# Performance work log

Measured on AMD Instinct MI355X. Metric: run time of the kernel, lower is better.

The kernel has to match this reference:

```python
import jax, jax.numpy as jnp
import numpy as np

B, N, D, H = 4, 2048, 1024, 16
DH = D // H


def setup_inputs() -> dict:
    key = jax.random.key(0)
    k_x, k_q, k_k, k_v, k_o = jax.random.split(key, 5)
    s = 1.0 / np.sqrt(D)
    return {
        "x": jax.random.normal(k_x, (B, N, D), dtype=jnp.float32),
        "mask": jnp.ones((B, N), dtype=bool),
        "Wq": jax.random.normal(k_q, (D, D), dtype=jnp.float32) * s,
        "Wk": jax.random.normal(k_k, (D, D), dtype=jnp.float32) * s,
        "Wv": jax.random.normal(k_v, (D, D), dtype=jnp.float32) * s,
        "Wo": jax.random.normal(k_o, (D, D), dtype=jnp.float32) * s,
    }


def reference(x, mask, Wq, Wk, Wv, Wo):
    # nn.Linear(bias=False): y = x @ W.T ; weights stored [out, in]
    q = jnp.einsum("bnd,ed->bne", x, Wq)
    k = jnp.einsum("bnd,ed->bne", x, Wk)
    v = jnp.einsum("bnd,ed->bne", x, Wv)
    # split heads: [b, n, d] -> [b, h, n, dh]
    def split(t):
        return t.reshape(B, N, H, DH).transpose(0, 2, 1, 3)
    q, k, v = split(q), split(k), split(v)
    # naive scaled dot-product attention (mask is dead code in the source)
    scores = jnp.einsum("bhnd,bhmd->bhnm", q, k) / jnp.sqrt(jnp.float32(DH))
    attn = jax.nn.softmax(scores, axis=-1)
    out = jnp.einsum("bhnm,bhmd->bhnd", attn, v)  # [b, h, n, dh]
    # merge heads: [b, h, n, dh] -> [b, n, d]
    out = out.transpose(0, 2, 1, 3).reshape(B, N, D)
    return jnp.einsum("bnd,ed->bne", out, Wo)
```

## Files before the change

kernel.cpp:

```cpp
#include <hip/hip_runtime.h>
#include <math.h>

constexpr int Bc  = 4;
constexpr int Nc  = 2048;
constexpr int Dc  = 1024;
constexpr int Hc  = 16;
constexpr int DHc = 64;
constexpr int Mrows = Bc * Nc;

typedef unsigned short ushortT;
typedef __attribute__((ext_vector_type(8))) short bf16x8;
typedef __attribute__((ext_vector_type(4))) unsigned short u16x4;
typedef __attribute__((ext_vector_type(4))) float f32x4;

#define QSCALE 0.18033688011112043f

#define GLD_LDS16(g, l)                                                        \
  __builtin_amdgcn_global_load_lds(                                            \
      (const __attribute__((address_space(1))) void*)(g),                      \
      (__attribute__((address_space(3))) void*)(l), 16, 0, 0)

__device__ inline ushortT f2bf(float f) {
  unsigned int u = __float_as_uint(f);
  u += 0x7fffu + ((u >> 16) & 1u);
  return (ushortT)(u >> 16);
}

__device__ inline float fexp2(float x) { return __builtin_amdgcn_exp2f(x); }

__global__ __launch_bounds__(256) void cvt_kernel(
    const float* __restrict__ x, const float* __restrict__ wq,
    const float* __restrict__ wk, const float* __restrict__ wv,
    const float* __restrict__ wo, ushortT* __restrict__ dst) {
  const int g = blockIdx.x * 256 + threadIdx.x;
  const float* src;
  size_t soff, doff;
  if (g < 2097152) {
    src = x;
    soff = (size_t)g * 4;
    doff = soff;
  } else {
    const int t = g - 2097152;
    const int w = t >> 18;
    const int off = t & 262143;
    src = (w == 0) ? wq : (w == 1) ? wk : (w == 2) ? wv : wo;
    soff = (size_t)off * 4;
    doff = 8388608u + (size_t)w * 1048576u + (size_t)off * 4;
  }
  float4 v = *(const float4*)(src + soff);
  ushort4 o = make_ushort4(f2bf(v.x), f2bf(v.y), f2bf(v.z), f2bf(v.w));
  *(ushort4*)(dst + doff) = o;
}

template <int QKV>
__global__ __launch_bounds__(256) void mfma_gemm(const ushortT* __restrict__ A,
                                                 const ushortT* __restrict__ W0,
                                                 void* __restrict__ C0) {
  __shared__ ushortT As[2][128 * 32];
  __shared__ ushortT Bs[2][128 * 32];

  const int tid = threadIdx.x;
  const int wave = tid >> 6, lane = tid & 63;
  const int quad = lane >> 4, lrow = lane & 15;
  const int bx = blockIdx.x, by = blockIdx.y;
  const int wsel = QKV ? (bx >> 3) : 0;
  const int e0 = QKV ? ((bx & 7) * 128) : (bx * 128);
  const int m0 = by * 128;
  const ushortT* Wp = W0 + (size_t)wsel * (Dc * Dc);
  const float oscale = (QKV && wsel == 0) ? QSCALE : 1.0f;

  const ushortT* ag = A  + (size_t)(m0 + wave * 32 + (lane >> 2)) * Dc + (lane & 3) * 8;
  const ushortT* bg = Wp + (size_t)(e0 + wave * 32 + (lane >> 2)) * Dc + (lane & 3) * 8;
  const int lbase = wave * 1024 + lane * 8;

  f32x4 acc[4][4];
#pragma unroll
  for (int i = 0; i < 4; ++i)
#pragma unroll
    for (int j = 0; j < 4; ++j) acc[i][j] = (f32x4){0.f, 0.f, 0.f, 0.f};

  const int wm = (wave >> 1) * 64, wn = (wave & 1) * 64;

  for (int k0 = 0; k0 < Dc; k0 += 64) {
    __syncthreads();
#pragma unroll
    for (int p = 0; p < 2; ++p) {
      GLD_LDS16(ag + p * 32, &As[p][lbase]);
      GLD_LDS16(ag + p * 32 + 16 * Dc, &As[p][lbase + 512]);
      GLD_LDS16(bg + p * 32, &Bs[p][lbase]);
      GLD_LDS16(bg + p * 32 + 16 * Dc, &Bs[p][lbase + 512]);
    }
    ag += 64;
    bg += 64;
    __syncthreads();

#pragma unroll
    for (int p = 0; p < 2; ++p) {
      bf16x8 af[4], bf[4];
#pragma unroll
      for (int mt = 0; mt < 4; ++mt)
        af[mt] = *(const bf16x8*)(&As[p][(wm + mt * 16 + lrow) * 32 + quad * 8]);
#pragma unroll
      for (int nt = 0; nt < 4; ++nt)
        bf[nt] = *(const bf16x8*)(&Bs[p][(wn + nt * 16 + lrow) * 32 + quad * 8]);
#pragma unroll
      for (int mt = 0; mt < 4; ++mt)
#pragma unroll
        for (int nt = 0; nt < 4; ++nt)
          acc[mt][nt] = __builtin_amdgcn_mfma_f32_16x16x32_bf16(
              af[mt], bf[nt], acc[mt][nt], 0, 0, 0);
    }
  }

#pragma unroll
  for (int mt = 0; mt < 4; ++mt) {
#pragma unroll
    for (int nt = 0; nt < 4; ++nt) {
#pragma unroll
      for (int r = 0; r < 4; ++r) {
        const int m = m0 + wm + mt * 16 + quad * 4 + r;
        const int e = e0 + wn + nt * 16 + lrow;
        const float v = acc[mt][nt][r] * oscale;
        if (QKV) {
          const int b = m >> 11, n = m & 2047;
          const int h = e >> 6, dh = e & 63;
          ushortT* C = (ushortT*)C0 + (size_t)wsel * ((size_t)Mrows * Dc);
          C[(((size_t)(b * Hc + h)) * Nc + n) * DHc + dh] = f2bf(v);
        } else {
          ((float*)C0)[(size_t)m * Dc + e] = v;
        }
      }
    }
  }
}

__global__ __launch_bounds__(256, 2) void attn_mfma(const ushortT* __restrict__ Q,
                                                    const ushortT* __restrict__ K,
                                                    const ushortT* __restrict__ V,
                                                    ushortT* __restrict__ O) {
  __shared__ ushortT smemA[256 * 72];
  __shared__ ushortT Ks[2][64 * 64];
  __shared__ ushortT Vt[64 * 72];

  const int tid = threadIdx.x;
  const int wave = tid >> 6, lane = tid & 63;
  const int quad = lane >> 4, lrow = lane & 15;
  const int bh = blockIdx.y;
  const int q0 = blockIdx.x * 256;

  const ushortT* qg = Q + (size_t)bh * Nc * DHc;
  const ushortT* kg = K + (size_t)bh * Nc * DHc;
  const ushortT* vg = V + (size_t)bh * Nc * DHc;

  const int kq = tid & 15;
  const int dhg = (tid >> 4) * 4;

#pragma unroll
  for (int c = 0; c < 2; ++c)
#pragma unroll
    for (int rh = 0; rh < 4; ++rh) {
      const int row = wave * 64 + rh * 16;
      GLD_LDS16(qg + (size_t)(q0 + row + (lane >> 2)) * DHc + c * 32 + (lane & 3) * 8,
                smemA + (c * 256 + row) * 32 + lane * 8);
    }
#pragma unroll
  for (int i = 0; i < 2; ++i) {
    const int cid = wave * 2 + i;
    const int c = cid & 1, kb = (cid >> 1) * 16;
    GLD_LDS16(kg + (size_t)(kb + (lane >> 2)) * DHc + c * 32 + (lane & 3) * 8,
              &Ks[0][(c * 64 + kb) * 32 + lane * 8]);
  }
  u16x4 vreg[4];
#pragma unroll
  for (int g = 0; g < 4; ++g)
    vreg[g] = *(const u16x4*)(vg + (size_t)(kq + 16 * g) * DHc + dhg);

  __syncthreads();

  bf16x8 af_q[4][2];
#pragma unroll
  for (int mt = 0; mt < 4; ++mt)
#pragma unroll
    for (int ks = 0; ks < 2; ++ks)
      af_q[mt][ks] = *(const bf16x8*)(smemA +
          ((ks * 256 + wave * 64 + mt * 16 + lrow) * 32 + quad * 8));

  {
    ushortT tmp[4][4];
#pragma unroll
    for (int g = 0; g < 4; ++g)
#pragma unroll
      for (int d = 0; d < 4; ++d) tmp[d][g] = vreg[g][d];
#pragma unroll
    for (int d = 0; d < 4; ++d)
      *(u16x4*)(Vt + (dhg + d) * 72 + kq * 4) = *(const u16x4*)tmp[d];
  }
  __syncthreads();

  f32x4 o_acc[4][4];
#pragma unroll
  for (int mt = 0; mt < 4; ++mt)
#pragma unroll
    for (int nt = 0; nt < 4; ++nt) o_acc[mt][nt] = (f32x4){0.f, 0.f, 0.f, 0.f};
  float l_i[16];
#pragma unroll
  for (int i = 0; i < 16; ++i) l_i[i] = 0.f;

  for (int k0 = 0; k0 < Nc; k0 += 64) {
    const int cur = (k0 >> 6) & 1, nxt = cur ^ 1;
    const bool pref = (k0 + 64 < Nc);

    if (pref) {
#pragma unroll
      for (int i = 0; i < 2; ++i) {
        const int cid = wave * 2 + i;
        const int c = cid & 1, kb = (cid >> 1) * 16;
        GLD_LDS16(kg + (size_t)(k0 + 64 + kb + (lane >> 2)) * DHc + c * 32 + (lane & 3) * 8,
                  &Ks[nxt][(c * 64 + kb) * 32 + lane * 8]);
      }
#pragma unroll
      for (int g = 0; g < 4; ++g)
        vreg[g] = *(const u16x4*)(vg + (size_t)(k0 + 64 + kq + 16 * g) * DHc + dhg);
    }

    bf16x8 bf_k[4][2];
#pragma unroll
    for (int nt = 0; nt < 4; ++nt)
#pragma unroll
      for (int ks = 0; ks < 2; ++ks)
        bf_k[nt][ks] = *(const bf16x8*)(&Ks[cur][(ks * 64 + nt * 16 + lrow) * 32 + quad * 8]);

    f32x4 s_acc[4][4];
#pragma unroll
    for (int mt = 0; mt < 4; ++mt)
#pragma unroll
      for (int nt = 0; nt < 4; ++nt) {
        s_acc[mt][nt] = (f32x4){0.f, 0.f, 0.f, 0.f};
#pragma unroll
        for (int ks = 0; ks < 2; ++ks)
          s_acc[mt][nt] = __builtin_amdgcn_mfma_f32_16x16x32_bf16(
              af_q[mt][ks], bf_k[nt][ks], s_acc[mt][nt], 0, 0, 0);
      }

#pragma unroll
    for (int mt = 0; mt < 4; ++mt) {
#pragma unroll
      for (int r = 0; r < 4; ++r) {
        const float p0 = fexp2(s_acc[mt][0][r]);
        const float p1 = fexp2(s_acc[mt][1][r]);
        const float p2 = fexp2(s_acc[mt][2][r]);
        const float p3 = fexp2(s_acc[mt][3][r]);
        l_i[mt * 4 + r] += (p0 + p1) + (p2 + p3);
        const unsigned pk01 = __builtin_amdgcn_perm(
            __float_as_uint(p1), __float_as_uint(p0), 0x07060302u);
        const unsigned pk23 = __builtin_amdgcn_perm(
            __float_as_uint(p3), __float_as_uint(p2), 0x07060302u);
        const int row = wave * 64 + mt * 16 + quad * 4 + r;
        *(uint2*)(smemA + row * 72 + lrow * 4) = make_uint2(pk01, pk23);
      }
    }
    asm volatile("s_waitcnt lgkmcnt(0)" ::: "memory");

    bf16x8 af_p[4][2], bf_v[4][2];
#pragma unroll
    for (int mt = 0; mt < 4; ++mt)
#pragma unroll
      for (int ks = 0; ks < 2; ++ks)
        af_p[mt][ks] = *(const bf16x8*)(smemA +
            (wave * 64 + mt * 16 + lrow) * 72 + ks * 32 + quad * 8);
#pragma unroll
    for (int nt = 0; nt < 4; ++nt)
#pragma unroll
      for (int ks = 0; ks < 2; ++ks)
        bf_v[nt][ks] = *(const bf16x8*)(Vt + (nt * 16 + lrow) * 72 + ks * 32 + quad * 8);
#pragma unroll
    for (int mt = 0; mt < 4; ++mt)
#pragma unroll
      for (int nt = 0; nt < 4; ++nt)
#pragma unroll
        for (int ks = 0; ks < 2; ++ks)
          o_acc[mt][nt] = __builtin_amdgcn_mfma_f32_16x16x32_bf16(
              af_p[mt][ks], bf_v[nt][ks], o_acc[mt][nt], 0, 0, 0);

    __syncthreads();

    if (pref) {
      ushortT tmp[4][4];
#pragma unroll
      for (int g = 0; g < 4; ++g)
#pragma unroll
        for (int d = 0; d < 4; ++d) tmp[d][g] = vreg[g][d];
#pragma unroll
      for (int d = 0; d < 4; ++d)
        *(u16x4*)(Vt + (dhg + d) * 72 + kq * 4) = *(const u16x4*)tmp[d];
    }

    __syncthreads();
  }

#pragma unroll
  for (int i = 0; i < 16; ++i) {
    float s = l_i[i];
#pragma unroll
    for (int off = 8; off >= 1; off >>= 1) s += __shfl_xor(s, off, 16);
    l_i[i] = s;
  }

  const int b = bh / Hc, h = bh % Hc;
#pragma unroll
  for (int mt = 0; mt < 4; ++mt) {
#pragma unroll
    for (int r = 0; r < 4; ++r) {
      const float inv_l = 1.0f / l_i[mt * 4 + r];
      const int n = q0 + wave * 64 + mt * 16 + quad * 4 + r;
      const size_t base = ((size_t)b * Nc + n) * Dc + h * DHc;
#pragma unroll
      for (int nt = 0; nt < 4; ++nt)
        O[base + nt * 16 + lrow] = f2bf(o_acc[mt][nt][r] * inv_l);
    }
  }
}

extern "C" void kernel_launch(void* const* d_in, const int* in_sizes, int n_in,
                              void* d_out, int out_size, void* d_ws,
                              size_t ws_size, hipStream_t stream) {
  const float* x  = (const float*)d_in[0];
  const float* Wq = (const float*)d_in[2];
  const float* Wk = (const float*)d_in[3];
  const float* Wv = (const float*)d_in[4];
  const float* Wo = (const float*)d_in[5];

  ushortT* ws16 = (ushortT*)d_ws;
  ushortT* xb   = ws16;
  ushortT* wqb  = xb + (size_t)Mrows * Dc;
  ushortT* qkvb = wqb + 4 * (size_t)Dc * Dc;
  ushortT* qb   = qkvb;
  ushortT* kb   = qb + (size_t)Mrows * Dc;
  ushortT* vb   = kb + (size_t)Mrows * Dc;
  ushortT* aob  = vb + (size_t)Mrows * Dc;
  ushortT* wob  = wqb + 3 * (size_t)Dc * Dc;

  dim3 blk(256);
  hipLaunchKernelGGL(cvt_kernel, dim3(12288), blk, 0, stream, x, Wq, Wk, Wv, Wo,
                     ws16);

  hipLaunchKernelGGL((mfma_gemm<1>), dim3(24, Mrows / 128), blk, 0, stream, xb,
                     wqb, (void*)qkvb);

  hipLaunchKernelGGL(attn_mfma, dim3(Nc / 256, Bc * Hc), blk, 0, stream, qb,
                     kb, vb, aob);

  hipLaunchKernelGGL((mfma_gemm<0>), dim3(8, Mrows / 128), blk, 0, stream, aob,
                     wob, d_out);
}
```

Measured before the change: 276.5 us.

## Swizzle GEMM grid, add MFMA priority hints, XOR-swizzle K LDS, double-buffer Vt

Remaps GEMM workgroup IDs so consecutive blocks share tiles, which is meant to improve L2 reuse. It also wraps the MFMA loops in s_setprio to favour matrix issue. In attention, K is loaded into LDS with an XOR swizzle to cut bank conflicts, and Vt is double-buffered so one __syncthreads per key tile can be dropped. The double buffer uses extra LDS, which may lower occupancy, and the swizzle has to match exactly between the global-to-LDS load and the LDS read.

```diff
diff --git a/kernel.cpp b/kernel.cpp
--- a/kernel.cpp
+++ b/kernel.cpp
@@ -62,7 +62,13 @@
   const int tid = threadIdx.x;
   const int wave = tid >> 6, lane = tid & 63;
   const int quad = lane >> 4, lrow = lane & 15;
-  const int bx = blockIdx.x, by = blockIdx.y;
+
+  const int gx = gridDim.x;
+  const int nwg = gx * gridDim.y;
+  const int orig = blockIdx.y * gx + blockIdx.x;
+  const int swz = (orig & 7) * (nwg >> 3) + (orig >> 3);
+  const int bx = swz % gx, by = swz / gx;
+
   const int wsel = QKV ? (bx >> 3) : 0;
   const int e0 = QKV ? ((bx & 7) * 128) : (bx * 128);
   const int m0 = by * 128;
@@ -103,12 +109,14 @@
 #pragma unroll
       for (int nt = 0; nt < 4; ++nt)
         bf[nt] = *(const bf16x8*)(&Bs[p][(wn + nt * 16 + lrow) * 32 + quad * 8]);
+      __builtin_amdgcn_s_setprio(1);
 #pragma unroll
       for (int mt = 0; mt < 4; ++mt)
 #pragma unroll
         for (int nt = 0; nt < 4; ++nt)
           acc[mt][nt] = __builtin_amdgcn_mfma_f32_16x16x32_bf16(
               af[mt], bf[nt], acc[mt][nt], 0, 0, 0);
+      __builtin_amdgcn_s_setprio(0);
     }
   }
 
@@ -140,7 +148,7 @@
                                                     ushortT* __restrict__ O) {
   __shared__ ushortT smemA[256 * 72];
   __shared__ ushortT Ks[2][64 * 64];
-  __shared__ ushortT Vt[64 * 72];
+  __shared__ ushortT Vt[2][64 * 72];
 
   const int tid = threadIdx.x;
   const int wave = tid >> 6, lane = tid & 63;
@@ -152,6 +160,9 @@
   const ushortT* kg = K + (size_t)bh * Nc * DHc;
   const ushortT* vg = V + (size_t)bh * Nc * DHc;
 
+  const int ksw = (lane & 3) ^ ((lane >> 3) & 3);
+  const int krd = (lrow >> 1) & 3;
+
   const int kq = tid & 15;
   const int dhg = (tid >> 4) * 4;
 
@@ -167,7 +178,7 @@
   for (int i = 0; i < 2; ++i) {
     const int cid = wave * 2 + i;
     const int c = cid & 1, kb = (cid >> 1) * 16;
-    GLD_LDS16(kg + (size_t)(kb + (lane >> 2)) * DHc + c * 32 + (lane & 3) * 8,
+    GLD_LDS16(kg + (size_t)(kb + (lane >> 2)) * DHc + c * 32 + ksw * 8,
               &Ks[0][(c * 64 + kb) * 32 + lane * 8]);
   }
   u16x4 vreg[4];
@@ -193,7 +204,7 @@
       for (int d = 0; d < 4; ++d) tmp[d][g] = vreg[g][d];
 #pragma unroll
     for (int d = 0; d < 4; ++d)
-      *(u16x4*)(Vt + (dhg + d) * 72 + kq * 4) = *(const u16x4*)tmp[d];
+      *(u16x4*)(&Vt[0][(dhg + d) * 72 + kq * 4]) = *(const u16x4*)tmp[d];
   }
   __syncthreads();
 
@@ -215,7 +226,7 @@
       for (int i = 0; i < 2; ++i) {
         const int cid = wave * 2 + i;
         const int c = cid & 1, kb = (cid >> 1) * 16;
-        GLD_LDS16(kg + (size_t)(k0 + 64 + kb + (lane >> 2)) * DHc + c * 32 + (lane & 3) * 8,
+        GLD_LDS16(kg + (size_t)(k0 + 64 + kb + (lane >> 2)) * DHc + c * 32 + ksw * 8,
                   &Ks[nxt][(c * 64 + kb) * 32 + lane * 8]);
       }
 #pragma unroll
@@ -228,9 +239,11 @@
     for (int nt = 0; nt < 4; ++nt)
 #pragma unroll
       for (int ks = 0; ks < 2; ++ks)
-        bf_k[nt][ks] = *(const bf16x8*)(&Ks[cur][(ks * 64 + nt * 16 + lrow) * 32 + quad * 8]);
+        bf_k[nt][ks] = *(const bf16x8*)(
+            &Ks[cur][(ks * 64 + nt * 16 + lrow) * 32 + (quad ^ krd) * 8]);
 
     f32x4 s_acc[4][4];
+    __builtin_amdgcn_s_setprio(1);
 #pragma unroll
     for (int mt = 0; mt < 4; ++mt)
 #pragma unroll
@@ -241,6 +254,7 @@
           s_acc[mt][nt] = __builtin_amdgcn_mfma_f32_16x16x32_bf16(
               af_q[mt][ks], bf_k[nt][ks], s_acc[mt][nt], 0, 0, 0);
       }
+    __builtin_amdgcn_s_setprio(0);
 
 #pragma unroll
     for (int mt = 0; mt < 4; ++mt) {
@@ -272,7 +286,9 @@
     for (int nt = 0; nt < 4; ++nt)
 #pragma unroll
       for (int ks = 0; ks < 2; ++ks)
-        bf_v[nt][ks] = *(const bf16x8*)(Vt + (nt * 16 + lrow) * 72 + ks * 32 + quad * 8);
+        bf_v[nt][ks] = *(const bf16x8*)(
+            &Vt[cur][(nt * 16 + lrow) * 72 + ks * 32 + quad * 8]);
+    __builtin_amdgcn_s_setprio(1);
 #pragma unroll
     for (int mt = 0; mt < 4; ++mt)
 #pragma unroll
@@ -281,8 +297,7 @@
         for (int ks = 0; ks < 2; ++ks)
           o_acc[mt][nt] = __builtin_amdgcn_mfma_f32_16x16x32_bf16(
               af_p[mt][ks], bf_v[nt][ks], o_acc[mt][nt], 0, 0, 0);
-
-    __syncthreads();
+    __builtin_amdgcn_s_setprio(0);
 
     if (pref) {
       ushortT tmp[4][4];
@@ -292,7 +307,7 @@
         for (int d = 0; d < 4; ++d) tmp[d][g] = vreg[g][d];
 #pragma unroll
       for (int d = 0; d < 4; ++d)
-        *(u16x4*)(Vt + (dhg + d) * 72 + kq * 4) = *(const u16x4*)tmp[d];
+        *(u16x4*)(&Vt[nxt][(dhg + d) * 72 + kq * 4]) = *(const u16x4*)tmp[d];
     }
 
     __syncthreads();
```

Result: slower. 297.6 us (+7.6%).
